# Kernel optimization log

Measured on AMD Instinct MI355X. Metric: run time of the kernel, lower is better.

Reference implementation:

```python
import jax, jax.numpy as jnp
import numpy as np

N = 100000        # num nodes
E = 1600000       # num directed edges (avg in-degree 16)
F = 128           # feature_dim
H = 128           # hidden_dim
SLOPE = 0.01      # leaky relu slope
ITERS = 3         # num_iterations (module default)


def _lrelu(v):
    return jnp.where(v >= 0, v, SLOPE * v)


def setup_inputs() -> dict:
    key = jax.random.key(0)
    ks = jax.random.split(key, 8)
    x = jax.random.normal(ks[0], (N, F), dtype=jnp.float32)
    edge_src = jax.random.randint(ks[1], (E,), 0, N, dtype=jnp.int32)
    edge_dst = jax.random.randint(ks[2], (E,), 0, N, dtype=jnp.int32)
    # Linear params (Kaiming-uniform-ish scale, like nn.Linear defaults)
    s1 = 1.0 / np.sqrt(F)
    s2 = 1.0 / np.sqrt(H)
    W1 = jax.random.uniform(ks[3], (F, H), jnp.float32, -s1, s1)
    b1 = jax.random.uniform(ks[4], (H,), jnp.float32, -s1, s1)
    W2 = jax.random.uniform(ks[5], (H, H), jnp.float32, -s2, s2)
    b2 = jax.random.uniform(ks[6], (H,), jnp.float32, -s2, s2)
    return {"x": x, "W1": W1, "b1": b1, "W2": W2, "b2": b2,
            "edge_src": edge_src, "edge_dst": edge_dst}


def reference(x, W1, b1, W2, b2, edge_src, edge_dst):
    # h_i = LeakyReLU(fc1(x_i))
    h = _lrelu(x @ W1 + b1)                                   # [N, H]
    # in-degree per node (neighbor count); zeros fallback for isolated nodes
    deg = jax.ops.segment_sum(jnp.ones((E,), x.dtype), edge_dst,
                              num_segments=N)                  # [N]
    inv = jnp.where(deg > 0, 1.0 / jnp.maximum(deg, 1.0), 0.0)[:, None]
    for _ in range(ITERS):
        # mean over neighbor embeddings (synchronous update, as in source)
        s = jax.ops.segment_sum(h[edge_src], edge_dst, num_segments=N)  # [N, H]
        m = s * inv                                            # [N, H]
        h = _lrelu(m @ W2 + b2 + h)
    return h
```

## Files before the change

### kernel.cpp

```cpp
#include <hip/hip_runtime.h>
#include <hip/hip_bf16.h>

#define N_NODES 100000
#define N_EDGES 1600000

#define BK_SHIFT 9
#define BK_NODES 512
#define NBKT 196
#define EDGES_PER_BLK 8192
#define NBLK_EDGE ((N_EDGES + EDGES_PER_BLK - 1) / EDGES_PER_BLK)

typedef unsigned short ush8 __attribute__((ext_vector_type(8)));
typedef __bf16 bf8 __attribute__((ext_vector_type(8)));
typedef float f4 __attribute__((ext_vector_type(4)));

__device__ __forceinline__ float lrelu(float v) {
    return v >= 0.0f ? v : 0.01f * v;
}

__device__ __forceinline__ unsigned short f2bf(float f) {
    unsigned u = __builtin_bit_cast(unsigned, f);
    return (unsigned short)((u + 0x7FFFu + ((u >> 16) & 1u)) >> 16);
}


__global__ __launch_bounds__(256) void bucket_count(const int* __restrict__ dst,
                                                    int* __restrict__ bcnt) {
    __shared__ int h[NBKT];
    int t = threadIdx.x;
    for (int i = t; i < NBKT; i += 256) h[i] = 0;
    __syncthreads();
    int base = blockIdx.x * EDGES_PER_BLK;
#pragma unroll 4
    for (int k = 0; k < EDGES_PER_BLK / 256; ++k) {
        int e = base + k * 256 + t;
        if (e < N_EDGES) atomicAdd(&h[dst[e] >> BK_SHIFT], 1);
    }
    __syncthreads();
    for (int i = t; i < NBKT; i += 256)
        if (h[i]) atomicAdd(&bcnt[i], h[i]);
}

__global__ void scan_buckets(const int* __restrict__ bcnt, int* __restrict__ boff,
                             int* __restrict__ bcur, int* __restrict__ off) {
    __shared__ int lds[256];
    int t = threadIdx.x;
    int v = (t < NBKT) ? bcnt[t] : 0;
    lds[t] = v;
    __syncthreads();
    for (int d = 1; d < 256; d <<= 1) {
        int a = (t >= d) ? lds[t - d] : 0;
        __syncthreads();
        lds[t] += a;
        __syncthreads();
    }
    if (t < NBKT) {
        int excl = lds[t] - v;
        boff[t] = excl;
        bcur[t] = excl;
    }
    if (t == 0) {
        boff[NBKT] = N_EDGES;
        off[N_NODES] = N_EDGES;
    }
}

__global__ __launch_bounds__(256) void bucket_scatter(const int* __restrict__ src,
                                                      const int* __restrict__ dst,
                                                      int* __restrict__ bcur,
                                                      unsigned* __restrict__ binned) {
    __shared__ int h[NBKT];
    __shared__ int bbase[NBKT];
    int t = threadIdx.x;
    for (int i = t; i < NBKT; i += 256) h[i] = 0;
    __syncthreads();
    int base = blockIdx.x * EDGES_PER_BLK;
#pragma unroll 4
    for (int k = 0; k < EDGES_PER_BLK / 256; ++k) {
        int e = base + k * 256 + t;
        if (e < N_EDGES) atomicAdd(&h[dst[e] >> BK_SHIFT], 1);
    }
    __syncthreads();
    for (int i = t; i < NBKT; i += 256) {
        int c = h[i];
        bbase[i] = c ? atomicAdd(&bcur[i], c) : 0;
        h[i] = 0;
    }
    __syncthreads();
#pragma unroll 4
    for (int k = 0; k < EDGES_PER_BLK / 256; ++k) {
        int e = base + k * 256 + t;
        if (e < N_EDGES) {
            int d = dst[e], s = src[e];
            int b = d >> BK_SHIFT;
            int p = bbase[b] + atomicAdd(&h[b], 1);
            binned[p] = ((unsigned)s << BK_SHIFT) | (unsigned)(d & (BK_NODES - 1));
        }
    }
}

__global__ __launch_bounds__(256) void bucket_place(const unsigned* __restrict__ binned,
                                                    const int* __restrict__ boff,
                                                    int* __restrict__ off,
                                                    int* __restrict__ csr) {
    __shared__ int hist[BK_NODES];
    __shared__ int pair[256];
    int b = blockIdx.x, t = threadIdx.x;
    int e0 = boff[b], e1 = boff[b + 1];
    hist[t] = 0;
    hist[t + 256] = 0;
    __syncthreads();
    for (int e = e0 + t; e < e1; e += 256)
        atomicAdd(&hist[binned[e] & (BK_NODES - 1)], 1);
    __syncthreads();
    int h0 = hist[2 * t], h1 = hist[2 * t + 1];
    pair[t] = h0 + h1;
    __syncthreads();
    for (int d = 1; d < 256; d <<= 1) {
        int a = (t >= d) ? pair[t - d] : 0;
        __syncthreads();
        pair[t] += a;
        __syncthreads();
    }
    int ep = pair[t] - (h0 + h1);
    int ex0 = ep, ex1 = ep + h0;
    int node0 = b * BK_NODES + 2 * t;
    if (node0 < N_NODES) off[node0] = e0 + ex0;
    if (node0 + 1 < N_NODES) off[node0 + 1] = e0 + ex1;
    __syncthreads();
    hist[2 * t] = ex0;
    hist[2 * t + 1] = ex1;
    __syncthreads();
    for (int e = e0 + t; e < e1; e += 256) {
        unsigned v = binned[e];
        int dl = v & (BK_NODES - 1);
        int p = atomicAdd(&hist[dl], 1);
        csr[e0 + p] = (int)(v >> BK_SHIFT);
    }
}


__global__ void wcast(const float* __restrict__ W1, const float* __restrict__ W2,
                      unsigned short* __restrict__ W1T, unsigned short* __restrict__ W2T) {
    int i = blockIdx.x * 256 + threadIdx.x;
    if (i >= 2 * 16384) return;
    const float* W = (i < 16384) ? W1 : W2;
    unsigned short* T = (i < 16384) ? W1T : W2T;
    int ii = i & 16383;
    int j = ii >> 7, k = ii & 127;
    T[ii] = f2bf(W[k * 128 + j]);
}

template <bool A_F32, bool RES, bool WB16>
__global__ __launch_bounds__(256) void gemm_fused(
    const void* __restrict__ Av, const unsigned short* __restrict__ WT,
    const float* __restrict__ bias, const float* __restrict__ res,
    float* __restrict__ outF, unsigned short* __restrict__ outB) {
    __shared__ unsigned short wlds[128][136];
    const int tid = threadIdx.x;
#pragma unroll
    for (int it = 0; it < 8; ++it) {
        int idx = it * 256 + tid;
        int r = idx >> 4, c = (idx & 15) << 3;
        *reinterpret_cast<ush8*>(&wlds[r][c]) =
            *reinterpret_cast<const ush8*>(&WT[r * 128 + c]);
    }
    __syncthreads();

    const int lane = tid & 63, wave = tid >> 6;
    const int row0 = blockIdx.x * 64 + wave * 16;
    const int rl = lane & 15, kg = lane >> 4;
    int arow = row0 + rl;
    if (arow >= N_NODES) arow = N_NODES - 1;

    bf8 af[4];
    if (A_F32) {
        const float* A = (const float*)Av;
#pragma unroll
        for (int kk = 0; kk < 4; ++kk) {
            const float* p = &A[arow * 128 + kk * 32 + kg * 8];
            float4 f0 = *reinterpret_cast<const float4*>(p);
            float4 f1 = *reinterpret_cast<const float4*>(p + 4);
            ush8 v;
            v[0] = f2bf(f0.x); v[1] = f2bf(f0.y); v[2] = f2bf(f0.z); v[3] = f2bf(f0.w);
            v[4] = f2bf(f1.x); v[5] = f2bf(f1.y); v[6] = f2bf(f1.z); v[7] = f2bf(f1.w);
            af[kk] = __builtin_bit_cast(bf8, v);
        }
    } else {
        const unsigned short* A = (const unsigned short*)Av;
#pragma unroll
        for (int kk = 0; kk < 4; ++kk)
            af[kk] = __builtin_bit_cast(
                bf8, *reinterpret_cast<const ush8*>(&A[arow * 128 + kk * 32 + kg * 8]));
    }

    f4 acc[8];
#pragma unroll
    for (int jt = 0; jt < 8; ++jt) acc[jt] = (f4)(0.0f);

#pragma unroll
    for (int jt = 0; jt < 8; ++jt) {
#pragma unroll
        for (int kk = 0; kk < 4; ++kk) {
            bf8 bfr = __builtin_bit_cast(
                bf8, *reinterpret_cast<const ush8*>(&wlds[jt * 16 + rl][kk * 32 + kg * 8]));
            acc[jt] = __builtin_amdgcn_mfma_f32_16x16x32_bf16(af[kk], bfr, acc[jt], 0, 0, 0);
        }
    }

#pragma unroll
    for (int jt = 0; jt < 8; ++jt) {
        int col = jt * 16 + rl;
        float bcol = bias[col];
#pragma unroll
        for (int i = 0; i < 4; ++i) {
            int r = row0 + kg * 4 + i;
            if (r < N_NODES) {
                float v = acc[jt][i] + bcol;
                if (RES) v += res[r * 128 + col];
                v = lrelu(v);
                outF[r * 128 + col] = v;
                if (WB16) outB[r * 128 + col] = f2bf(v);
            }
        }
    }
}

__global__ __launch_bounds__(256) void agg_kernel(
    const unsigned short* __restrict__ h, const int* __restrict__ off,
    const int* __restrict__ csr, unsigned short* __restrict__ m) {
    int row = blockIdx.x * 4 + (threadIdx.x >> 6);
    if (row >= N_NODES) return;
    int lane = threadIdx.x & 63;
    int e0 = off[row], e1 = off[row + 1];
    const unsigned* hb = reinterpret_cast<const unsigned*>(h);
    float ax = 0.0f, ay = 0.0f;
    int e = e0;
    for (; e + 8 <= e1; e += 8) {
        int s[8];
#pragma unroll
        for (int k = 0; k < 8; ++k) s[k] = csr[e + k];
#pragma unroll
        for (int k = 0; k < 8; ++k) {
            unsigned u = hb[s[k] * 64 + lane];
            ax += __builtin_bit_cast(float, u << 16);
            ay += __builtin_bit_cast(float, u & 0xFFFF0000u);
        }
    }
    for (; e + 2 <= e1; e += 2) {
        unsigned u0 = hb[csr[e] * 64 + lane];
        unsigned u1 = hb[csr[e + 1] * 64 + lane];
        ax += __builtin_bit_cast(float, u0 << 16) + __builtin_bit_cast(float, u1 << 16);
        ay += __builtin_bit_cast(float, u0 & 0xFFFF0000u) +
              __builtin_bit_cast(float, u1 & 0xFFFF0000u);
    }
    if (e < e1) {
        unsigned u = hb[csr[e] * 64 + lane];
        ax += __builtin_bit_cast(float, u << 16);
        ay += __builtin_bit_cast(float, u & 0xFFFF0000u);
    }
    int d = e1 - e0;
    float inv = (d > 0) ? 1.0f / (float)d : 0.0f;
    unsigned pk = ((unsigned)f2bf(ay * inv) << 16) | (unsigned)f2bf(ax * inv);
    reinterpret_cast<unsigned*>(m)[row * 64 + lane] = pk;
}


extern "C" void kernel_launch(void* const* d_in, const int* in_sizes, int n_in,
                              void* d_out, int out_size, void* d_ws, size_t ws_size,
                              hipStream_t stream) {
    const float* x  = (const float*)d_in[0];
    const float* W1 = (const float*)d_in[1];
    const float* b1 = (const float*)d_in[2];
    const float* W2 = (const float*)d_in[3];
    const float* b2 = (const float*)d_in[4];
    const int* esrc = (const int*)d_in[5];
    const int* edst = (const int*)d_in[6];
    float* out = (float*)d_out;

    char* ws = (char*)d_ws;
    size_t o = 0;
    auto alloc = [&](size_t b) {
        void* p = ws + o;
        o += (b + 511) & ~(size_t)511;
        return p;
    };
    int* bcnt = (int*)alloc(NBKT * 4);
    int* boff = (int*)alloc((NBKT + 1) * 4);
    int* bcur = (int*)alloc(NBKT * 4);
    int* off  = (int*)alloc(((size_t)N_NODES + 1) * 4);
    int* csr  = (int*)alloc((size_t)N_EDGES * 4);
    unsigned short* W1T = (unsigned short*)alloc(128 * 128 * 2);
    unsigned short* W2T = (unsigned short*)alloc(128 * 128 * 2);
    float* ha = (float*)alloc((size_t)N_NODES * 128 * 4);
    unsigned short* hB = (unsigned short*)alloc((size_t)N_NODES * 128 * 2);
    unsigned short* m  = (unsigned short*)alloc((size_t)N_NODES * 128 * 2);
    unsigned* binned = (unsigned*)m;

    hipMemsetAsync(bcnt, 0, NBKT * 4, stream);
    bucket_count<<<NBLK_EDGE, 256, 0, stream>>>(edst, bcnt);
    scan_buckets<<<1, 256, 0, stream>>>(bcnt, boff, bcur, off);
    bucket_scatter<<<NBLK_EDGE, 256, 0, stream>>>(esrc, edst, bcur, binned);
    bucket_place<<<NBKT, 256, 0, stream>>>(binned, boff, off, csr);

    wcast<<<(2 * 16384 + 255) / 256, 256, 0, stream>>>(W1, W2, W1T, W2T);

    const int GB = (N_NODES + 63) / 64;
    gemm_fused<true, false, true><<<GB, 256, 0, stream>>>(x, W1T, b1, nullptr, ha, hB);

    agg_kernel<<<(N_NODES + 3) / 4, 256, 0, stream>>>(hB, off, csr, m);
    gemm_fused<false, true, true><<<GB, 256, 0, stream>>>(m, W2T, b2, ha, out, hB);
    agg_kernel<<<(N_NODES + 3) / 4, 256, 0, stream>>>(hB, off, csr, m);
    gemm_fused<false, true, true><<<GB, 256, 0, stream>>>(m, W2T, b2, out, ha, hB);
    agg_kernel<<<(N_NODES + 3) / 4, 256, 0, stream>>>(hB, off, csr, m);
    gemm_fused<false, true, false><<<GB, 256, 0, stream>>>(m, W2T, b2, ha, out, nullptr);
}
```

Baseline: 487.7 us.

## Keep hidden state in bf16 only, fold residual into MFMA, widen aggregation loads

Drops the fp32 copy of the hidden state. The residual is now read from the bf16 buffer and added inside the MFMA accumulator by multiplying with an identity B-fragment, and the W LDS barrier is moved after that work. The GEMM can now skip the fp32 output, so only the final layer writes fp32. The aggregation kernel splits each node's edges across two half-waves with 8-byte loads per lane and combines them with a cross-lane shuffle. This cuts per-layer fp32 read/write traffic, but the residual path now carries bf16 rounding error across iterations.

```diff
diff --git a/kernel.cpp b/kernel.cpp
--- a/kernel.cpp
+++ b/kernel.cpp
@@ -21,6 +21,13 @@
 __device__ __forceinline__ unsigned short f2bf(float f) {
     unsigned u = __builtin_bit_cast(unsigned, f);
     return (unsigned short)((u + 0x7FFFu + ((u >> 16) & 1u)) >> 16);
+}
+
+__device__ __forceinline__ float bfhi(unsigned u) {
+    return __builtin_bit_cast(float, u & 0xFFFF0000u);
+}
+__device__ __forceinline__ float bflo(unsigned u) {
+    return __builtin_bit_cast(float, u << 16);
 }
 
 
@@ -151,10 +158,10 @@
     T[ii] = f2bf(W[k * 128 + j]);
 }
 
-template <bool A_F32, bool RES, bool WB16>
+template <bool A_F32, bool RES, bool WF32, bool WB16>
 __global__ __launch_bounds__(256) void gemm_fused(
     const void* __restrict__ Av, const unsigned short* __restrict__ WT,
-    const float* __restrict__ bias, const float* __restrict__ res,
+    const float* __restrict__ bias, const unsigned short* __restrict__ resB,
     float* __restrict__ outF, unsigned short* __restrict__ outB) {
     __shared__ unsigned short wlds[128][136];
     const int tid = threadIdx.x;
@@ -165,7 +172,6 @@
         *reinterpret_cast<ush8*>(&wlds[r][c]) =
             *reinterpret_cast<const ush8*>(&WT[r * 128 + c]);
     }
-    __syncthreads();
 
     const int lane = tid & 63, wave = tid >> 6;
     const int row0 = blockIdx.x * 64 + wave * 16;
@@ -198,6 +204,23 @@
 #pragma unroll
     for (int jt = 0; jt < 8; ++jt) acc[jt] = (f4)(0.0f);
 
+    if (RES) {
+        ush8 bi;
+#pragma unroll
+        for (int j = 0; j < 8; ++j)
+            bi[j] = (kg * 8 + j == rl) ? (unsigned short)0x3F80 : (unsigned short)0;
+        bf8 bfi = __builtin_bit_cast(bf8, bi);
+#pragma unroll
+        for (int jt = 0; jt < 8; ++jt) {
+            bf8 ra = __builtin_bit_cast(
+                bf8, *reinterpret_cast<const ush8*>(
+                         &resB[arow * 128 + jt * 16 + (kg & 1) * 8]));
+            acc[jt] = __builtin_amdgcn_mfma_f32_16x16x32_bf16(ra, bfi, acc[jt], 0, 0, 0);
+        }
+    }
+
+    __syncthreads();
+
 #pragma unroll
     for (int jt = 0; jt < 8; ++jt) {
 #pragma unroll
@@ -217,9 +240,8 @@
             int r = row0 + kg * 4 + i;
             if (r < N_NODES) {
                 float v = acc[jt][i] + bcol;
-                if (RES) v += res[r * 128 + col];
                 v = lrelu(v);
-                outF[r * 128 + col] = v;
+                if (WF32) outF[r * 128 + col] = v;
                 if (WB16) outB[r * 128 + col] = f2bf(v);
             }
         }
@@ -232,37 +254,41 @@
     int row = blockIdx.x * 4 + (threadIdx.x >> 6);
     if (row >= N_NODES) return;
     int lane = threadIdx.x & 63;
+    int half = lane >> 5, hl = lane & 31;
     int e0 = off[row], e1 = off[row + 1];
-    const unsigned* hb = reinterpret_cast<const unsigned*>(h);
-    float ax = 0.0f, ay = 0.0f;
-    int e = e0;
+    const uint2* hb = reinterpret_cast<const uint2*>(h);
+    float a0 = 0.f, a1 = 0.f, a2 = 0.f, a3 = 0.f;
+    int e = e0 + half;
     for (; e + 8 <= e1; e += 8) {
-        int s[8];
-#pragma unroll
-        for (int k = 0; k < 8; ++k) s[k] = csr[e + k];
-#pragma unroll
-        for (int k = 0; k < 8; ++k) {
-            unsigned u = hb[s[k] * 64 + lane];
-            ax += __builtin_bit_cast(float, u << 16);
-            ay += __builtin_bit_cast(float, u & 0xFFFF0000u);
-        }
-    }
-    for (; e + 2 <= e1; e += 2) {
-        unsigned u0 = hb[csr[e] * 64 + lane];
-        unsigned u1 = hb[csr[e + 1] * 64 + lane];
-        ax += __builtin_bit_cast(float, u0 << 16) + __builtin_bit_cast(float, u1 << 16);
-        ay += __builtin_bit_cast(float, u0 & 0xFFFF0000u) +
-              __builtin_bit_cast(float, u1 & 0xFFFF0000u);
-    }
-    if (e < e1) {
-        unsigned u = hb[csr[e] * 64 + lane];
-        ax += __builtin_bit_cast(float, u << 16);
-        ay += __builtin_bit_cast(float, u & 0xFFFF0000u);
-    }
+        int s0 = csr[e], s1 = csr[e + 2], s2 = csr[e + 4], s3 = csr[e + 6];
+        uint2 v0 = hb[s0 * 32 + hl];
+        uint2 v1 = hb[s1 * 32 + hl];
+        uint2 v2 = hb[s2 * 32 + hl];
+        uint2 v3 = hb[s3 * 32 + hl];
+        a0 += bflo(v0.x) + bflo(v1.x) + bflo(v2.x) + bflo(v3.x);
+        a1 += bfhi(v0.x) + bfhi(v1.x) + bfhi(v2.x) + bfhi(v3.x);
+        a2 += bflo(v0.y) + bflo(v1.y) + bflo(v2.y) + bflo(v3.y);
+        a3 += bfhi(v0.y) + bfhi(v1.y) + bfhi(v2.y) + bfhi(v3.y);
+    }
+    for (; e < e1; e += 2) {
+        uint2 v = hb[csr[e] * 32 + hl];
+        a0 += bflo(v.x);
+        a1 += bfhi(v.x);
+        a2 += bflo(v.y);
+        a3 += bfhi(v.y);
+    }
+    a0 += __shfl_xor(a0, 32);
+    a1 += __shfl_xor(a1, 32);
+    a2 += __shfl_xor(a2, 32);
+    a3 += __shfl_xor(a3, 32);
     int d = e1 - e0;
     float inv = (d > 0) ? 1.0f / (float)d : 0.0f;
-    unsigned pk = ((unsigned)f2bf(ay * inv) << 16) | (unsigned)f2bf(ax * inv);
-    reinterpret_cast<unsigned*>(m)[row * 64 + lane] = pk;
+    if (half == 0) {
+        uint2 pk;
+        pk.x = ((unsigned)f2bf(a1 * inv) << 16) | (unsigned)f2bf(a0 * inv);
+        pk.y = ((unsigned)f2bf(a3 * inv) << 16) | (unsigned)f2bf(a2 * inv);
+        reinterpret_cast<uint2*>(m)[row * 32 + hl] = pk;
+    }
 }
 
 
@@ -292,7 +318,6 @@
     int* csr  = (int*)alloc((size_t)N_EDGES * 4);
     unsigned short* W1T = (unsigned short*)alloc(128 * 128 * 2);
     unsigned short* W2T = (unsigned short*)alloc(128 * 128 * 2);
-    float* ha = (float*)alloc((size_t)N_NODES * 128 * 4);
     unsigned short* hB = (unsigned short*)alloc((size_t)N_NODES * 128 * 2);
     unsigned short* m  = (unsigned short*)alloc((size_t)N_NODES * 128 * 2);
     unsigned* binned = (unsigned*)m;
@@ -306,12 +331,15 @@
     wcast<<<(2 * 16384 + 255) / 256, 256, 0, stream>>>(W1, W2, W1T, W2T);
 
     const int GB = (N_NODES + 63) / 64;
-    gemm_fused<true, false, true><<<GB, 256, 0, stream>>>(x, W1T, b1, nullptr, ha, hB);
-
+    gemm_fused<true, false, false, true><<<GB, 256, 0, stream>>>(
+        x, W1T, b1, nullptr, nullptr, hB);
+
+    for (int it = 0; it < 2; ++it) {
+        agg_kernel<<<(N_NODES + 3) / 4, 256, 0, stream>>>(hB, off, csr, m);
+        gemm_fused<false, true, false, true><<<GB, 256, 0, stream>>>(
+            m, W2T, b2, hB, nullptr, hB);
+    }
     agg_kernel<<<(N_NODES + 3) / 4, 256, 0, stream>>>(hB, off, csr, m);
-    gemm_fused<false, true, true><<<GB, 256, 0, stream>>>(m, W2T, b2, ha, out, hB);
-    agg_kernel<<<(N_NODES + 3) / 4, 256, 0, stream>>>(hB, off, csr, m);
-    gemm_fused<false, true, true><<<GB, 256, 0, stream>>>(m, W2T, b2, out, ha, hB);
-    agg_kernel<<<(N_NODES + 3) / 4, 256, 0, stream>>>(hB, off, csr, m);
-    gemm_fused<false, true, false><<<GB, 256, 0, stream>>>(m, W2T, b2, ha, out, nullptr);
-}
+    gemm_fused<false, true, true, false><<<GB, 256, 0, stream>>>(
+        m, W2T, b2, hB, out, nullptr);
+}
```

Measured after the change: 478.0 us. 2.0% less time.

## Keep hidden state in bf16 only, vectorize GEMM epilogue via permuted W2

Applied to the files above, without the earlier changes.

Drops the fp32 hidden-state buffer. Intermediate layers now write only bf16 h, and the residual is read back from that bf16 copy, which cuts epilogue memory traffic. W2 is pre-permuted so each lane's 8 output columns map to contiguous bf16 addresses, allowing 16-byte residual loads and stores. The A-tile load is also moved ahead of the LDS barrier, and a 16-wide gather unroll is added to the aggregation loop. The cost is that the residual path now runs in bf16, which adds rounding error against the fp32 reference.

```diff
diff --git a/kernel.cpp b/kernel.cpp
--- a/kernel.cpp
+++ b/kernel.cpp
@@ -21,6 +21,15 @@
 __device__ __forceinline__ unsigned short f2bf(float f) {
     unsigned u = __builtin_bit_cast(unsigned, f);
     return (unsigned short)((u + 0x7FFFu + ((u >> 16) & 1u)) >> 16);
+}
+__device__ __forceinline__ float bfs(unsigned short u) {
+    return __builtin_bit_cast(float, (unsigned)u << 16);
+}
+__device__ __forceinline__ float bfhi(unsigned u) {
+    return __builtin_bit_cast(float, u & 0xFFFF0000u);
+}
+__device__ __forceinline__ float bflo(unsigned u) {
+    return __builtin_bit_cast(float, u << 16);
 }
 
 
@@ -139,22 +148,24 @@
     }
 }
 
-
 __global__ void wcast(const float* __restrict__ W1, const float* __restrict__ W2,
                       unsigned short* __restrict__ W1T, unsigned short* __restrict__ W2T) {
     int i = blockIdx.x * 256 + threadIdx.x;
     if (i >= 2 * 16384) return;
-    const float* W = (i < 16384) ? W1 : W2;
-    unsigned short* T = (i < 16384) ? W1T : W2T;
     int ii = i & 16383;
-    int j = ii >> 7, k = ii & 127;
-    T[ii] = f2bf(W[k * 128 + j]);
-}
-
-template <bool A_F32, bool RES, bool WB16>
+    int col = ii >> 7, q = ii & 127;
+    if (i < 16384) {
+        W1T[ii] = f2bf(W1[q * 128 + col]);
+    } else {
+        int k = 16 * (q & 7) + (q >> 3);
+        W2T[ii] = f2bf(W2[k * 128 + col]);
+    }
+}
+
+template <bool A_F32, bool RES, bool FINAL>
 __global__ __launch_bounds__(256) void gemm_fused(
     const void* __restrict__ Av, const unsigned short* __restrict__ WT,
-    const float* __restrict__ bias, const float* __restrict__ res,
+    const float* __restrict__ bias, const unsigned short* __restrict__ resB,
     float* __restrict__ outF, unsigned short* __restrict__ outB) {
     __shared__ unsigned short wlds[128][136];
     const int tid = threadIdx.x;
@@ -165,7 +176,6 @@
         *reinterpret_cast<ush8*>(&wlds[r][c]) =
             *reinterpret_cast<const ush8*>(&WT[r * 128 + c]);
     }
-    __syncthreads();
 
     const int lane = tid & 63, wave = tid >> 6;
     const int row0 = blockIdx.x * 64 + wave * 16;
@@ -194,6 +204,8 @@
                 bf8, *reinterpret_cast<const ush8*>(&A[arow * 128 + kk * 32 + kg * 8]));
     }
 
+    __syncthreads();
+
     f4 acc[8];
 #pragma unroll
     for (int jt = 0; jt < 8; ++jt) acc[jt] = (f4)(0.0f);
@@ -208,20 +220,35 @@
         }
     }
 
-#pragma unroll
-    for (int jt = 0; jt < 8; ++jt) {
-        int col = jt * 16 + rl;
-        float bcol = bias[col];
-#pragma unroll
-        for (int i = 0; i < 4; ++i) {
-            int r = row0 + kg * 4 + i;
+    float bb[8];
+#pragma unroll
+    for (int j = 0; j < 8; ++j) bb[j] = bias[j * 16 + rl];
+
+#pragma unroll
+    for (int i = 0; i < 4; ++i) {
+        int r = row0 + kg * 4 + i;
+        int rc = (r < N_NODES) ? r : N_NODES - 1;
+        ush8 rv;
+        if (RES)
+            rv = *reinterpret_cast<const ush8*>(&resB[rc * 128 + rl * 8]);
+        float v[8];
+#pragma unroll
+        for (int j = 0; j < 8; ++j) {
+            float t = acc[j][i] + bb[j];
+            if (RES) t += bfs(rv[j]);
+            v[j] = lrelu(t);
+        }
+        if (FINAL) {
             if (r < N_NODES) {
-                float v = acc[jt][i] + bcol;
-                if (RES) v += res[r * 128 + col];
-                v = lrelu(v);
-                outF[r * 128 + col] = v;
-                if (WB16) outB[r * 128 + col] = f2bf(v);
+#pragma unroll
+                for (int j = 0; j < 8; ++j) outF[r * 128 + j * 16 + rl] = v[j];
             }
+        } else {
+            ush8 sv;
+#pragma unroll
+            for (int j = 0; j < 8; ++j) sv[j] = f2bf(v[j]);
+            if (r < N_NODES)
+                *reinterpret_cast<ush8*>(&outB[r * 128 + rl * 8]) = sv;
         }
     }
 }
@@ -236,6 +263,17 @@
     const unsigned* hb = reinterpret_cast<const unsigned*>(h);
     float ax = 0.0f, ay = 0.0f;
     int e = e0;
+    for (; e + 16 <= e1; e += 16) {
+        int s[16];
+#pragma unroll
+        for (int k = 0; k < 16; ++k) s[k] = csr[e + k];
+#pragma unroll
+        for (int k = 0; k < 16; ++k) {
+            unsigned u = hb[s[k] * 64 + lane];
+            ax += __builtin_bit_cast(float, u << 16);
+            ay += __builtin_bit_cast(float, u & 0xFFFF0000u);
+        }
+    }
     for (; e + 8 <= e1; e += 8) {
         int s[8];
 #pragma unroll
@@ -292,7 +330,6 @@
     int* csr  = (int*)alloc((size_t)N_EDGES * 4);
     unsigned short* W1T = (unsigned short*)alloc(128 * 128 * 2);
     unsigned short* W2T = (unsigned short*)alloc(128 * 128 * 2);
-    float* ha = (float*)alloc((size_t)N_NODES * 128 * 4);
     unsigned short* hB = (unsigned short*)alloc((size_t)N_NODES * 128 * 2);
     unsigned short* m  = (unsigned short*)alloc((size_t)N_NODES * 128 * 2);
     unsigned* binned = (unsigned*)m;
@@ -306,12 +343,15 @@
     wcast<<<(2 * 16384 + 255) / 256, 256, 0, stream>>>(W1, W2, W1T, W2T);
 
     const int GB = (N_NODES + 63) / 64;
-    gemm_fused<true, false, true><<<GB, 256, 0, stream>>>(x, W1T, b1, nullptr, ha, hB);
-
+    gemm_fused<true, false, false><<<GB, 256, 0, stream>>>(
+        x, W1T, b1, nullptr, nullptr, hB);
+
+    for (int it = 0; it < 2; ++it) {
+        agg_kernel<<<(N_NODES + 3) / 4, 256, 0, stream>>>(hB, off, csr, m);
+        gemm_fused<false, true, false><<<GB, 256, 0, stream>>>(
+            m, W2T, b2, hB, nullptr, hB);
+    }
     agg_kernel<<<(N_NODES + 3) / 4, 256, 0, stream>>>(hB, off, csr, m);
-    gemm_fused<false, true, true><<<GB, 256, 0, stream>>>(m, W2T, b2, ha, out, hB);
-    agg_kernel<<<(N_NODES + 3) / 4, 256, 0, stream>>>(hB, off, csr, m);
-    gemm_fused<false, true, true><<<GB, 256, 0, stream>>>(m, W2T, b2, out, ha, hB);
-    agg_kernel<<<(N_NODES + 3) / 4, 256, 0, stream>>>(hB, off, csr, m);
-    gemm_fused<false, true, false><<<GB, 256, 0, stream>>>(m, W2T, b2, ha, out, nullptr);
-}
+    gemm_fused<false, true, true><<<GB, 256, 0, stream>>>(
+        m, W2T, b2, hB, out, nullptr);
+}
```

Result: faster. 398.4 us (-18.3%).
